# Optimization experiments

Hardware: AMD Instinct MI355X
Metric: run time of the kernel (lower is better)

## Reference

```python
import jax, jax.numpy as jnp
import numpy as np

B, N, D, H, L = 8, 1025, 1024, 8, 2   # N = maxlen + 1
NUM_BUCKETS = 64
EPS = 1e-8


def layernorm(x):
    mu = jnp.mean(x, axis=-1, keepdims=True)
    var = jnp.mean((x - mu) ** 2, axis=-1, keepdims=True)
    return (x - mu) / jnp.sqrt(var + EPS)


def rmsnorm(x):
    return x * jax.lax.rsqrt(jnp.mean(x * x, axis=-1, keepdims=True) + EPS)


def rel_attn_bias(action_ts, ts_w, pos_w):
    # positional part: pos_w[j - i + N - 1]  (equivalent to the pad/repeat trick)
    idx = jnp.arange(N)[None, :] - jnp.arange(N)[:, None] + (N - 1)  # [N,N] in [0,2N-2]
    rel_pos = pos_w[idx][None]  # [1,N,N]
    # time part: bucketize ext[i+1] - ext[j], ext = cat(ts, ts[:, N-1:N])
    ext = jnp.concatenate([action_ts, action_ts[:, N - 1:N]], axis=1)  # [B,N+1]
    diff = ext[:, 1:, None] - ext[:, None, :-1]  # [B,N,N]
    bucket = (jnp.log(jnp.clip(jnp.abs(diff), 1, None).astype(jnp.float32)) / 0.301).astype(jnp.int32)
    bucket = jnp.clip(bucket, 0, NUM_BUCKETS)
    rel_ts = ts_w[bucket]  # [B,N,N]
    return rel_pos + rel_ts


def hstu_block(x, mask, bias, qkvu, out_w, out_b, fc1_w, fc1_b, fc2_w, fc2_b):
    hd = D // H
    xn = layernorm(x)
    qkvu_act = jax.nn.silu(xn @ qkvu)  # [B,N,4D]
    q, k, v, u = jnp.split(qkvu_act, 4, axis=-1)
    q = q.reshape(B, N, H, hd)
    k = k.reshape(B, N, H, hd)
    v = v.reshape(B, N, H, hd)
    scores = jnp.einsum('bihd,bjhd->bhij', q, k) + bias[:, None]  # [B,H,N,N]
    attn = jax.nn.silu(scores) / N * mask[:, None]
    av = jnp.einsum('bhij,bjhd->bihd', attn, v).reshape(B, N, D)
    attn_out = (u * layernorm(av)) @ out_w + out_b
    h = x + attn_out
    # SwiGLU FFN (mult=2) with RMSNorm pre-norm and residual
    vg = rmsnorm(h) @ fc1_w + fc1_b  # [B,N,4D]
    vv, g = jnp.split(vg, 2, axis=-1)
    y = (jax.nn.silu(g) * vv) @ fc2_w + fc2_b
    return h + y


def setup_inputs() -> dict:
    key = jax.random.key(0)
    ks = jax.random.split(key, 12)
    std = 0.02
    seqs = jax.random.normal(ks[0], (B, N, D), jnp.float32)
    mask = jnp.tril(jnp.ones((N, N), jnp.float32))[None].repeat(B, axis=0)
    action_ts = jnp.sort(jax.random.randint(ks[1], (B, N), 0, 1000000000).astype(jnp.int64), axis=1)
    return {
        'seqs': seqs,
        'mask': mask,
        'action_ts': action_ts,
        'qkvu': jax.random.normal(ks[2], (L, D, 4 * D), jnp.float32) * std,
        'out_w': jax.random.normal(ks[3], (L, D, D), jnp.float32) * std,
        'out_b': jnp.zeros((L, D), jnp.float32),
        'ts_w': jax.random.normal(ks[4], (L, NUM_BUCKETS + 1), jnp.float32) * std,
        'pos_w': jax.random.normal(ks[5], (L, 2 * N - 1), jnp.float32) * std,
        'fc1_w': jax.random.normal(ks[6], (L, D, 4 * D), jnp.float32) * std,
        'fc1_b': jnp.zeros((L, 4 * D), jnp.float32),
        'fc2_w': jax.random.normal(ks[7], (L, 2 * D, D), jnp.float32) * std,
        'fc2_b': jnp.zeros((L, D), jnp.float32),
    }


def reference(seqs, mask, action_ts, qkvu, out_w, out_b, ts_w, pos_w, fc1_w, fc1_b, fc2_w, fc2_b):
    h = seqs
    for l in range(L):
        bias = rel_attn_bias(action_ts, ts_w[l], pos_w[l])
        h = hstu_block(h, mask, bias, qkvu[l], out_w[l], out_b[l],
                       fc1_w[l], fc1_b[l], fc2_w[l], fc2_b[l])
    return h
```

## Files before the change

kernel.cpp:

```cpp
#include <hip/hip_runtime.h>
#include <hip/hip_bf16.h>
#include <math.h>

#define BB 8
#define SEQN 1025
#define DD 1024
#define HH 8
#define HD 128
#define LL 2
#define MROWS (BB*SEQN)
#define MPAD 8320
#define NBUCKET 64

using short8 = __attribute__((ext_vector_type(8))) short;
using f32x4  = __attribute__((ext_vector_type(4))) float;
using f32x16 = __attribute__((ext_vector_type(16))) float;

__device__ __forceinline__ float silu_f(float x) { return x / (1.f + expf(-x)); }

__device__ __forceinline__ float bf2f(ushort u) {
  union { uint i; float f; } x; x.i = ((uint)u) << 16; return x.f;
}
__device__ __forceinline__ ushort f2bf(float f) {
  __hip_bfloat16 b = __float2bfloat16(f);
  return *reinterpret_cast<ushort*>(&b);
}
__device__ __forceinline__ void gll16(const void* g, void* l) {
  __builtin_amdgcn_global_load_lds((const __attribute__((address_space(1))) void*)g,
                                   (__attribute__((address_space(3))) void*)l, 16, 0, 0);
}
__device__ __forceinline__ uint pkbf(float lo, float hi) {
  uint r;
  asm("v_cvt_pk_bf16_f32 %0, %1, %2" : "=v"(r) : "v"(lo), "v"(hi));
  return r;
}
__device__ __forceinline__ f32x16 z16() {
  f32x16 v;
#pragma unroll
  for (int i = 0; i < 16; ++i) v[i] = 0.f;
  return v;
}

__global__ __launch_bounds__(256) void copy_kernel(const float* __restrict__ in,
                                                   float* __restrict__ out, int n4) {
  int idx = blockIdx.x * blockDim.x + threadIdx.x;
  int stride = gridDim.x * blockDim.x;
  const float4* i4 = (const float4*)in;
  float4* o4 = (float4*)out;
  for (int i = idx; i < n4; i += stride) o4[i] = i4[i];
}

__global__ __launch_bounds__(256) void wtrans(const float* __restrict__ W,
                                              ushort* __restrict__ Wt, int K, int N) {
  __shared__ float tile[32][33];
  int tid = threadIdx.x;
  int tx = tid & 31, ty = tid >> 5;
  int n0 = blockIdx.x * 32, k0 = blockIdx.y * 32;
#pragma unroll
  for (int r = 0; r < 32; r += 8)
    tile[ty + r][tx] = W[(size_t)(k0 + ty + r) * N + n0 + tx];
  __syncthreads();
#pragma unroll
  for (int r = 0; r < 32; r += 8)
    Wt[(size_t)(n0 + ty + r) * K + k0 + tx] = f2bf(tile[tx][ty + r]);
}

__global__ __launch_bounds__(256) void bias_kernel(const int* __restrict__ ts,
    const float* __restrict__ ts_w, const float* __restrict__ pos_w,
    float* __restrict__ biasT)
{
  int i = blockIdx.x * 256 + threadIdx.x;
  int j = blockIdx.y;
  int b = blockIdx.z;
  if (i >= SEQN) return;
  int ip1 = i + 1; if (ip1 > SEQN - 1) ip1 = SEQN - 1;
  long long t1 = (long long)ts[b * SEQN + ip1];
  long long t0 = (long long)ts[b * SEQN + j];
  long long d = t1 - t0;
  if (d < 0) d = -d;
  if (d < 1) d = 1;
  int bucket = (int)(logf((float)d) / 0.301f);
  if (bucket < 0) bucket = 0;
  if (bucket > NBUCKET) bucket = NBUCKET;
  biasT[((size_t)(b * SEQN + j)) * SEQN + i] = pos_w[j - i + SEQN - 1] + ts_w[bucket];
}

__global__ __launch_bounds__(256) void ln_kernel(const float* __restrict__ in,
                                                 ushort* __restrict__ out) {
  int row = blockIdx.x;
  int tid = threadIdx.x;
  const float* x = in + (size_t)row * DD;
  float4 v = *(const float4*)&x[tid * 4];
  float s = v.x + v.y + v.z + v.w;
  float ss = v.x*v.x + v.y*v.y + v.z*v.z + v.w*v.w;
#pragma unroll
  for (int off = 32; off >= 1; off >>= 1) { s += __shfl_xor(s, off); ss += __shfl_xor(ss, off); }
  __shared__ float red0[4], red1[4];
  if ((tid & 63) == 0) { red0[tid >> 6] = s; red1[tid >> 6] = ss; }
  __syncthreads();
  s = red0[0] + red0[1] + red0[2] + red0[3];
  ss = red1[0] + red1[1] + red1[2] + red1[3];
  float mu = s * (1.f / DD);
  float var = fmaxf(ss * (1.f / DD) - mu * mu, 0.f);
  float inv = 1.f / sqrtf(var + 1e-8f);
  ushort4 o;
  o.x = f2bf((v.x - mu) * inv); o.y = f2bf((v.y - mu) * inv);
  o.z = f2bf((v.z - mu) * inv); o.w = f2bf((v.w - mu) * inv);
  *(ushort4*)&out[(size_t)row * DD + tid * 4] = o;
}

__global__ __launch_bounds__(256) void rms_kernel(const float* __restrict__ in,
                                                  ushort* __restrict__ out) {
  int row = blockIdx.x;
  int tid = threadIdx.x;
  const float* x = in + (size_t)row * DD;
  float4 v = *(const float4*)&x[tid * 4];
  float ss = v.x*v.x + v.y*v.y + v.z*v.z + v.w*v.w;
#pragma unroll
  for (int off = 32; off >= 1; off >>= 1) ss += __shfl_xor(ss, off);
  __shared__ float red1[4];
  if ((tid & 63) == 0) red1[tid >> 6] = ss;
  __syncthreads();
  ss = red1[0] + red1[1] + red1[2] + red1[3];
  float inv = 1.f / sqrtf(ss * (1.f / DD) + 1e-8f);
  ushort4 o;
  o.x = f2bf(v.x * inv); o.y = f2bf(v.y * inv);
  o.z = f2bf(v.z * inv); o.w = f2bf(v.w * inv);
  *(ushort4*)&out[(size_t)row * DD + tid * 4] = o;
}

__global__ __launch_bounds__(256) void uln_kernel(const float* __restrict__ av,
    const ushort* __restrict__ act, ushort* __restrict__ out) {
  int row = blockIdx.x;
  int tid = threadIdx.x;
  const float* x = av + (size_t)row * DD;
  float4 v = *(const float4*)&x[tid * 4];
  float s = v.x + v.y + v.z + v.w;
  float ss = v.x*v.x + v.y*v.y + v.z*v.z + v.w*v.w;
#pragma unroll
  for (int off = 32; off >= 1; off >>= 1) { s += __shfl_xor(s, off); ss += __shfl_xor(ss, off); }
  __shared__ float red0[4], red1[4];
  if ((tid & 63) == 0) { red0[tid >> 6] = s; red1[tid >> 6] = ss; }
  __syncthreads();
  s = red0[0] + red0[1] + red0[2] + red0[3];
  ss = red1[0] + red1[1] + red1[2] + red1[3];
  float mu = s * (1.f / DD);
  float var = fmaxf(ss * (1.f / DD) - mu * mu, 0.f);
  float inv = 1.f / sqrtf(var + 1e-8f);
  ushort4 uu = *(const ushort4*)&act[(size_t)row * 4096 + 3072 + tid * 4];
  ushort4 o;
  o.x = f2bf(bf2f(uu.x) * (v.x - mu) * inv);
  o.y = f2bf(bf2f(uu.y) * (v.y - mu) * inv);
  o.z = f2bf(bf2f(uu.z) * (v.z - mu) * inv);
  o.w = f2bf(bf2f(uu.w) * (v.w - mu) * inv);
  *(ushort4*)&out[(size_t)row * DD + tid * 4] = o;
}

__global__ __launch_bounds__(256) void gated_kernel(const ushort* __restrict__ act,
                                                    ushort* __restrict__ gated) {
  int idx = blockIdx.x * 256 + threadIdx.x;
  const int total = MROWS * 2048 / 8;
  if (idx >= total) return;
  int row = idx >> 8;
  int col = (idx & 255) * 8;
  const ushort* base = act + (size_t)row * 4096;
  short8 vv = *(const short8*)(base + col);
  short8 gg = *(const short8*)(base + 2048 + col);
  short8 o;
#pragma unroll
  for (int j = 0; j < 8; ++j) {
    float v = bf2f((ushort)vv[j]);
    float g = bf2f((ushort)gg[j]);
    o[j] = (short)f2bf(silu_f(g) * v);
  }
  *(short8*)&gated[(size_t)row * 2048 + col] = o;
}

template<int MODE>
__global__ __launch_bounds__(256, 2) void mgemm(const ushort* __restrict__ A,
    const ushort* __restrict__ Bt, const float* __restrict__ bvec,
    void* __restrict__ Cout, int M, int Nn, int K)
{
  __shared__ ushort As[2][8192];
  __shared__ ushort Bs[2][8192];
  const int tid  = threadIdx.x;
  const int lane = tid & 63, wave = tid >> 6;
  const int wm = wave >> 1, wn = wave & 1;
  const int lrow = lane & 15, lk = lane >> 4;

  const int nwg = gridDim.x * gridDim.y;
  const int bid = blockIdx.y * gridDim.x + blockIdx.x;
  const int sw  = (bid & 7) * (nwg >> 3) + (bid >> 3);
  const int bm = (sw / gridDim.x) * 128, bn = (sw % gridDim.x) * 128;

  const ushort* Aga[4]; const ushort* Bga[4];
  ushort* Ada[4]; ushort* Bda[4];
#pragma unroll
  for (int i = 0; i < 4; ++i) {
    int c = tid + 256 * i;
    int row = c >> 3, s = c & 7;
    int sc = s ^ (row & 7);
    Aga[i] = A  + (size_t)(bm + row) * K + sc * 8;
    Bga[i] = Bt + (size_t)(bn + row) * K + sc * 8;
    Ada[i] = &As[0][c * 8];
    Bda[i] = &Bs[0][c * 8];
  }

  int aoff[2][4], boff[2][4];
#pragma unroll
  for (int kk = 0; kk < 2; ++kk) {
#pragma unroll
    for (int m = 0; m < 4; ++m)
      aoff[kk][m] = (wm * 64 + m * 16 + lrow) * 64 + (((kk * 4 + lk) ^ (lrow & 7)) * 8);
#pragma unroll
    for (int n = 0; n < 4; ++n)
      boff[kk][n] = (wn * 64 + n * 16 + lrow) * 64 + (((kk * 4 + lk) ^ (lrow & 7)) * 8);
  }

  f32x4 acc[4][4];
#pragma unroll
  for (int m = 0; m < 4; ++m)
#pragma unroll
    for (int n = 0; n < 4; ++n) acc[m][n] = (f32x4){0.f, 0.f, 0.f, 0.f};

  const int nk = K >> 6;
#pragma unroll
  for (int i = 0; i < 4; ++i) {
    gll16(Aga[i], Ada[i]);
    gll16(Bga[i], Bda[i]);
  }
  int buf = 0;
  for (int kt = 0; kt < nk; ++kt) {
    if (kt + 1 < nk) {
      const int ko = (kt + 1) << 6;
      const int bo = (buf ^ 1) * 8192;
#pragma unroll
      for (int i = 0; i < 4; ++i) {
        gll16(Aga[i] + ko, Ada[i] + bo);
        gll16(Bga[i] + ko, Bda[i] + bo);
      }
      asm volatile("s_waitcnt vmcnt(8)" ::: "memory");
    } else {
      asm volatile("s_waitcnt vmcnt(0)" ::: "memory");
    }
    __builtin_amdgcn_s_barrier();
    __builtin_amdgcn_sched_barrier(0);
    __builtin_amdgcn_s_setprio(1);
#pragma unroll
    for (int kk = 0; kk < 2; ++kk) {
      short8 af[4], bfr[4];
#pragma unroll
      for (int m = 0; m < 4; ++m) af[m]  = *(const short8*)&As[buf][aoff[kk][m]];
#pragma unroll
      for (int n = 0; n < 4; ++n) bfr[n] = *(const short8*)&Bs[buf][boff[kk][n]];
#pragma unroll
      for (int m = 0; m < 4; ++m)
#pragma unroll
        for (int n = 0; n < 4; ++n)
          acc[m][n] = __builtin_amdgcn_mfma_f32_16x16x32_bf16(af[m], bfr[n], acc[m][n], 0, 0, 0);
    }
    __builtin_amdgcn_s_setprio(0);
    __builtin_amdgcn_sched_barrier(0);
    __builtin_amdgcn_s_barrier();
    buf ^= 1;
  }

  const int colbase = bn + wn * 64 + lrow;
  const int rowbase = bm + wm * 64 + lk * 4;
  if (MODE == 1) {
    float* Cf = (float*)Cout;
#pragma unroll
    for (int m = 0; m < 4; ++m) {
      int row0 = rowbase + m * 16;
#pragma unroll
      for (int n = 0; n < 4; ++n) {
        int col = colbase + n * 16;
        float bv = bvec[col];
#pragma unroll
        for (int r = 0; r < 4; ++r) {
          int row = row0 + r;
          if (row < M) {
            float* p = Cf + (size_t)row * Nn + col;
            *p += acc[m][n][r] + bv;
          }
        }
      }
    }
  } else {
    __hip_bfloat16* Cb = (__hip_bfloat16*)Cout;
#pragma unroll
    for (int m = 0; m < 4; ++m) {
      int row0 = rowbase + m * 16;
#pragma unroll
      for (int n = 0; n < 4; ++n) {
        int col = colbase + n * 16;
        float bv = (MODE == 2) ? bvec[col] : 0.f;
#pragma unroll
        for (int r = 0; r < 4; ++r) {
          int row = row0 + r;
          if (row < M) {
            float v = acc[m][n][r];
            float o = (MODE == 0) ? silu_f(v) : (v + bv);
            Cb[(size_t)row * Nn + col] = __float2bfloat16(o);
          }
        }
      }
    }
  }
}

__global__ __launch_bounds__(256) void attn_kernel(const ushort* __restrict__ act,
    const float* __restrict__ biasT, float* __restrict__ av)
{
  __shared__ __align__(16) char KL[8192];
  __shared__ __align__(16) char VL[8320];
  const int tid = threadIdx.x;
  const int l = tid & 63, w = tid >> 6;
  const int qi = (int)(gridDim.x - 1 - blockIdx.x);
  const int i0 = qi * 128;
  const int h = blockIdx.y, b = blockIdx.z;
  const int lo31 = l & 31, hi = l >> 5;

  const int jlim = (i0 + 128 < SEQN) ? i0 + 128 : SEQN;
  const int nt = (jlim + 31) >> 5;

  const int gi_q = i0 + w * 32 + lo31;
  const int gi_qc = gi_q < SEQN ? gi_q : SEQN - 1;
  const size_t actB = (size_t)b * SEQN;
  const ushort* qrow = act + (actB + gi_qc) * 4096 + h * HD;
  short8 qreg[8];
#pragma unroll
  for (int dc = 0; dc < 8; ++dc)
    qreg[dc] = *(const short8*)(qrow + dc * 16 + hi * 8);

  f32x16 acc[4];
#pragma unroll
  for (int dt = 0; dt < 4; ++dt) acc[dt] = z16();

  const int id0 = tid, id1 = tid + 256;
  const int j_0 = id0 >> 4, c8_0 = (id0 & 15) * 8;
  const int j_1 = id1 >> 4, c8_1 = (id1 & 15) * 8;
  char* kw0 = KL + j_0 * 256 + (((id0 & 15) ^ (j_0 & 15)) << 4);
  char* kw1 = KL + j_1 * 256 + (((id1 & 15) ^ (j_1 & 15)) << 4);
  char* vw0 = VL + ((id0 & 15) >> 1) * 1040 + j_0 * 32 + (id0 & 1) * 16;
  char* vw1 = VL + ((id1 & 15) >> 1) * 1040 + j_1 * 32 + (id1 & 1) * 16;
  const uint vbase = (uint)(size_t)(__attribute__((address_space(3))) char*)
      (VL + ((l >> 4) & 1) * 1040 + hi * 256 + (l & 15) * 8);

  short8 kr0, kr1, vr0, vr1;
  {
    const ushort* p0 = act + (actB + j_0) * 4096 + 1024 + h * HD + c8_0;
    const ushort* p1 = act + (actB + j_1) * 4096 + 1024 + h * HD + c8_1;
    kr0 = *(const short8*)p0; vr0 = *(const short8*)(p0 + 1024);
    kr1 = *(const short8*)p1; vr1 = *(const short8*)(p1 + 1024);
  }
  const float invN = 1.f / (float)SEQN;
  const int gi0w = i0 + w * 32;

  for (int t = 0; t < nt; ++t) {
    const int j0 = t * 32;
    __syncthreads();
    *(short8*)kw0 = kr0; *(short8*)kw1 = kr1;
    *(short8*)vw0 = vr0; *(short8*)vw1 = vr1;
    __syncthreads();
    if (t + 1 < nt) {
      const ushort* p0 = act + (actB + j0 + 32 + j_0) * 4096 + 1024 + h * HD + c8_0;
      const ushort* p1 = act + (actB + j0 + 32 + j_1) * 4096 + 1024 + h * HD + c8_1;
      kr0 = *(const short8*)p0; vr0 = *(const short8*)(p0 + 1024);
      kr1 = *(const short8*)p1; vr1 = *(const short8*)(p1 + 1024);
    }
    if (j0 <= gi0w + 31 && gi0w < SEQN) {
      float bv[16];
#pragma unroll
      for (int r = 0; r < 16; ++r) {
        int j = (r & 3) + 8 * (r >> 2) + 4 * hi;
        int gj = j0 + j;
        int gjc = gj < SEQN ? gj : SEQN - 1;
        bv[r] = biasT[(actB + gjc) * SEQN + gi_qc];
      }
      f32x16 st = z16();
#pragma unroll
      for (int dc = 0; dc < 8; ++dc) {
        short8 kf = *(const short8*)(KL + lo31 * 256 + ((((dc << 1) + hi) ^ (lo31 & 15)) << 4));
        st = __builtin_amdgcn_mfma_f32_32x32x16_bf16(kf, qreg[dc], st, 0, 0, 0);
      }
      float p[16];
#pragma unroll
      for (int r = 0; r < 16; ++r) {
        int j = (r & 3) + 8 * (r >> 2) + 4 * hi;
        int gj = j0 + j;
        float s = st[r] + bv[r];
        float pw = s * __builtin_amdgcn_rcpf(1.f + __expf(-s)) * invN;
        p[r] = ((gj <= gi_q) && (gi_q < SEQN)) ? pw : 0.f;
      }
      short8 paf[2];
#pragma unroll
      for (int g = 0; g < 2; ++g) {
        uint w0 = pkbf(p[g * 8 + 0], p[g * 8 + 1]);
        uint w2 = pkbf(p[g * 8 + 4], p[g * 8 + 5]);
        uint w1 = pkbf(p[g * 8 + 2], p[g * 8 + 3]);
        uint w3 = pkbf(p[g * 8 + 6], p[g * 8 + 7]);
        asm volatile("v_permlane32_swap_b32 %0, %1" : "+v"(w0), "+v"(w2));
        asm volatile("v_permlane32_swap_b32 %0, %1" : "+v"(w1), "+v"(w3));
        union UF { uint u[4]; short8 s; } uf;
        uf.u[0] = w0; uf.u[1] = w1; uf.u[2] = w2; uf.u[3] = w3;
        paf[g] = uf.s;
      }
      uint64_t v00, v01, v02, v03, v10, v11, v12, v13, v20, v21, v22, v23, v30, v31, v32, v33;
      asm volatile(
        "ds_read_b64_tr_b16 %0, %16 offset:0\n\t"
        "ds_read_b64_tr_b16 %1, %16 offset:128\n\t"
        "ds_read_b64_tr_b16 %2, %16 offset:512\n\t"
        "ds_read_b64_tr_b16 %3, %16 offset:640\n\t"
        "ds_read_b64_tr_b16 %4, %16 offset:2080\n\t"
        "ds_read_b64_tr_b16 %5, %16 offset:2208\n\t"
        "ds_read_b64_tr_b16 %6, %16 offset:2592\n\t"
        "ds_read_b64_tr_b16 %7, %16 offset:2720\n\t"
        "ds_read_b64_tr_b16 %8, %16 offset:4160\n\t"
        "ds_read_b64_tr_b16 %9, %16 offset:4288\n\t"
        "ds_read_b64_tr_b16 %10, %16 offset:4672\n\t"
        "ds_read_b64_tr_b16 %11, %16 offset:4800\n\t"
        "ds_read_b64_tr_b16 %12, %16 offset:6240\n\t"
        "ds_read_b64_tr_b16 %13, %16 offset:6368\n\t"
        "ds_read_b64_tr_b16 %14, %16 offset:6752\n\t"
        "ds_read_b64_tr_b16 %15, %16 offset:6880\n\t"
        "s_waitcnt lgkmcnt(0)"
        : "=v"(v00), "=v"(v01), "=v"(v02), "=v"(v03),
          "=v"(v10), "=v"(v11), "=v"(v12), "=v"(v13),
          "=v"(v20), "=v"(v21), "=v"(v22), "=v"(v23),
          "=v"(v30), "=v"(v31), "=v"(v32), "=v"(v33)
        : "v"(vbase) : "memory");
      union UV { uint64_t q[2]; short8 s; };
      { UV uv; uv.q[0] = v00; uv.q[1] = v01;
        acc[0] = __builtin_amdgcn_mfma_f32_32x32x16_bf16(paf[0], uv.s, acc[0], 0, 0, 0); }
      { UV uv; uv.q[0] = v02; uv.q[1] = v03;
        acc[0] = __builtin_amdgcn_mfma_f32_32x32x16_bf16(paf[1], uv.s, acc[0], 0, 0, 0); }
      { UV uv; uv.q[0] = v10; uv.q[1] = v11;
        acc[1] = __builtin_amdgcn_mfma_f32_32x32x16_bf16(paf[0], uv.s, acc[1], 0, 0, 0); }
      { UV uv; uv.q[0] = v12; uv.q[1] = v13;
        acc[1] = __builtin_amdgcn_mfma_f32_32x32x16_bf16(paf[1], uv.s, acc[1], 0, 0, 0); }
      { UV uv; uv.q[0] = v20; uv.q[1] = v21;
        acc[2] = __builtin_amdgcn_mfma_f32_32x32x16_bf16(paf[0], uv.s, acc[2], 0, 0, 0); }
      { UV uv; uv.q[0] = v22; uv.q[1] = v23;
        acc[2] = __builtin_amdgcn_mfma_f32_32x32x16_bf16(paf[1], uv.s, acc[2], 0, 0, 0); }
      { UV uv; uv.q[0] = v30; uv.q[1] = v31;
        acc[3] = __builtin_amdgcn_mfma_f32_32x32x16_bf16(paf[0], uv.s, acc[3], 0, 0, 0); }
      { UV uv; uv.q[0] = v32; uv.q[1] = v33;
        acc[3] = __builtin_amdgcn_mfma_f32_32x32x16_bf16(paf[1], uv.s, acc[3], 0, 0, 0); }
    }
  }
#pragma unroll
  for (int dt = 0; dt < 4; ++dt) {
#pragma unroll
    for (int r = 0; r < 16; ++r) {
      int q = (r & 3) + 8 * (r >> 2) + 4 * hi;
      int gi = i0 + w * 32 + q;
      if (gi < SEQN)
        av[(actB + gi) * DD + h * HD + dt * 32 + lo31] = acc[dt][r];
    }
  }
}

extern "C" void kernel_launch(void* const* d_in, const int* in_sizes, int n_in,
                              void* d_out, int out_size, void* d_ws, size_t ws_size,
                              hipStream_t stream) {
  const float* seqs  = (const float*)d_in[0];
  const int*   ts    = (const int*)d_in[2];
  const float* qkvuW = (const float*)d_in[3];
  const float* outW  = (const float*)d_in[4];
  const float* outB  = (const float*)d_in[5];
  const float* tsW   = (const float*)d_in[6];
  const float* posW  = (const float*)d_in[7];
  const float* fc1W  = (const float*)d_in[8];
  const float* fc1B  = (const float*)d_in[9];
  const float* fc2W  = (const float*)d_in[10];
  const float* fc2B  = (const float*)d_in[11];
  float* h = (float*)d_out;
  char* ws = (char*)d_ws;

  ushort* xn    = (ushort*)(ws);
  ushort* act   = (ushort*)(ws + 17039360);
  ushort* gated = (ushort*)(ws + 85196800);
  float*  biasT = (float*) (ws + 119275520);
  float*  av    = (float*) (ws + 152895520);
  ushort* wq    = (ushort*)(ws + 186482720);
  ushort* wo    = (ushort*)(ws + 194871328);
  ushort* wf1   = (ushort*)(ws + 196968480);
  ushort* wf2   = (ushort*)(ws + 205357088);

  copy_kernel<<<2048, 256, 0, stream>>>(seqs, h, MROWS * DD / 4);

  for (int l = 0; l < LL; l++) {
    wtrans<<<dim3(128, 32), 256, 0, stream>>>(qkvuW + (size_t)l * DD * 4096, wq, DD, 4096);
    wtrans<<<dim3(32, 32),  256, 0, stream>>>(outW  + (size_t)l * DD * DD,   wo, DD, DD);
    wtrans<<<dim3(128, 32), 256, 0, stream>>>(fc1W  + (size_t)l * DD * 4096, wf1, DD, 4096);
    wtrans<<<dim3(32, 64),  256, 0, stream>>>(fc2W  + (size_t)l * 2048 * DD, wf2, 2048, DD);

    bias_kernel<<<dim3(5, SEQN, BB), 256, 0, stream>>>(
        ts, tsW + l * (NBUCKET + 1), posW + l * (2 * SEQN - 1), biasT);

    ln_kernel<<<MROWS, 256, 0, stream>>>(h, xn);
    mgemm<0><<<dim3(32, 65), 256, 0, stream>>>(xn, wq, nullptr, act, MROWS, 4096, DD);
    attn_kernel<<<dim3(9, HH, BB), 256, 0, stream>>>(act, biasT, av);
    uln_kernel<<<MROWS, 256, 0, stream>>>(av, act, xn);
    mgemm<1><<<dim3(8, 65), 256, 0, stream>>>(xn, wo, outB + l * DD, h, MROWS, DD, DD);
    rms_kernel<<<MROWS, 256, 0, stream>>>(h, xn);
    mgemm<2><<<dim3(32, 65), 256, 0, stream>>>(xn, wf1, fc1B + (size_t)l * 4096, act, MROWS, 4096, DD);
    gated_kernel<<<8200, 256, 0, stream>>>(act, gated);
    mgemm<1><<<dim3(8, 65), 256, 0, stream>>>(gated, wf2, fc2B + l * DD, h, MROWS, DD, 2048);
  }
}
```

Measured before the change: 1.239 ms.

## Switch GEMM to triple-buffered BK=32 pipeline with one barrier per iteration

Reworks the bf16 MFMA GEMM main loop from a double-buffered K-tile of 64 to a triple-buffered K-tile of 32, prefetching two stages ahead. The trailing barrier is dropped so each iteration syncs only once, and the LDS swizzle is adapted to the 32-wide rows. The block-id swizzle for L2 locality and the occupancy hint in launch_bounds are removed. Each iteration does half the MFMA work between barriers, so the barrier overhead per unit of work may rise. The LDS footprint shrinks, which could allow more workgroups per CU.

```diff
diff --git a/kernel.cpp b/kernel.cpp
--- a/kernel.cpp
+++ b/kernel.cpp
@@ -177,45 +177,38 @@
 }
 
 template<int MODE>
-__global__ __launch_bounds__(256, 2) void mgemm(const ushort* __restrict__ A,
+__global__ __launch_bounds__(256) void mgemm(const ushort* __restrict__ A,
     const ushort* __restrict__ Bt, const float* __restrict__ bvec,
     void* __restrict__ Cout, int M, int Nn, int K)
 {
-  __shared__ ushort As[2][8192];
-  __shared__ ushort Bs[2][8192];
+  __shared__ ushort As[3][4096];
+  __shared__ ushort Bs[3][4096];
   const int tid  = threadIdx.x;
   const int lane = tid & 63, wave = tid >> 6;
   const int wm = wave >> 1, wn = wave & 1;
   const int lrow = lane & 15, lk = lane >> 4;
-
-  const int nwg = gridDim.x * gridDim.y;
-  const int bid = blockIdx.y * gridDim.x + blockIdx.x;
-  const int sw  = (bid & 7) * (nwg >> 3) + (bid >> 3);
-  const int bm = (sw / gridDim.x) * 128, bn = (sw % gridDim.x) * 128;
-
-  const ushort* Aga[4]; const ushort* Bga[4];
-  ushort* Ada[4]; ushort* Bda[4];
-#pragma unroll
-  for (int i = 0; i < 4; ++i) {
+  const int bm = blockIdx.y * 128, bn = blockIdx.x * 128;
+
+  const ushort* Aga[2]; const ushort* Bga[2];
+  ushort* Ada[2]; ushort* Bda[2];
+#pragma unroll
+  for (int i = 0; i < 2; ++i) {
     int c = tid + 256 * i;
-    int row = c >> 3, s = c & 7;
-    int sc = s ^ (row & 7);
+    int row = c >> 2, s = c & 3;
+    int sc = s ^ ((row >> 1) & 3);
     Aga[i] = A  + (size_t)(bm + row) * K + sc * 8;
     Bga[i] = Bt + (size_t)(bn + row) * K + sc * 8;
     Ada[i] = &As[0][c * 8];
     Bda[i] = &Bs[0][c * 8];
   }
 
-  int aoff[2][4], boff[2][4];
-#pragma unroll
-  for (int kk = 0; kk < 2; ++kk) {
-#pragma unroll
-    for (int m = 0; m < 4; ++m)
-      aoff[kk][m] = (wm * 64 + m * 16 + lrow) * 64 + (((kk * 4 + lk) ^ (lrow & 7)) * 8);
-#pragma unroll
-    for (int n = 0; n < 4; ++n)
-      boff[kk][n] = (wn * 64 + n * 16 + lrow) * 64 + (((kk * 4 + lk) ^ (lrow & 7)) * 8);
-  }
+  int aoff[4], boff[4];
+#pragma unroll
+  for (int m = 0; m < 4; ++m)
+    aoff[m] = (wm * 64 + m * 16 + lrow) * 32 + ((lk ^ ((lrow >> 1) & 3)) * 8);
+#pragma unroll
+  for (int n = 0; n < 4; ++n)
+    boff[n] = (wn * 64 + n * 16 + lrow) * 32 + ((lk ^ ((lrow >> 1) & 3)) * 8);
 
   f32x4 acc[4][4];
 #pragma unroll
@@ -223,36 +216,41 @@
 #pragma unroll
     for (int n = 0; n < 4; ++n) acc[m][n] = (f32x4){0.f, 0.f, 0.f, 0.f};
 
-  const int nk = K >> 6;
-#pragma unroll
-  for (int i = 0; i < 4; ++i) {
-    gll16(Aga[i], Ada[i]);
-    gll16(Bga[i], Bda[i]);
-  }
-  int buf = 0;
+  const int nk = K >> 5;
+#pragma unroll
+  for (int t = 0; t < 2; ++t) {
+#pragma unroll
+    for (int i = 0; i < 2; ++i) {
+      gll16(Aga[i] + (t << 5), Ada[i] + t * 4096);
+      gll16(Bga[i] + (t << 5), Bda[i] + t * 4096);
+    }
+  }
+  int cur = 0, nxt2 = 2;
   for (int kt = 0; kt < nk; ++kt) {
     if (kt + 1 < nk) {
-      const int ko = (kt + 1) << 6;
-      const int bo = (buf ^ 1) * 8192;
-#pragma unroll
-      for (int i = 0; i < 4; ++i) {
+      asm volatile("s_waitcnt vmcnt(4)" ::: "memory");
+    } else {
+      asm volatile("s_waitcnt vmcnt(0)" ::: "memory");
+    }
+    __builtin_amdgcn_s_barrier();
+    __builtin_amdgcn_sched_barrier(0);
+    if (kt + 2 < nk) {
+      const int ko = (kt + 2) << 5;
+      const int bo = nxt2 * 4096;
+#pragma unroll
+      for (int i = 0; i < 2; ++i) {
         gll16(Aga[i] + ko, Ada[i] + bo);
         gll16(Bga[i] + ko, Bda[i] + bo);
       }
-      asm volatile("s_waitcnt vmcnt(8)" ::: "memory");
-    } else {
-      asm volatile("s_waitcnt vmcnt(0)" ::: "memory");
-    }
-    __builtin_amdgcn_s_barrier();
-    __builtin_amdgcn_sched_barrier(0);
+    }
     __builtin_amdgcn_s_setprio(1);
-#pragma unroll
-    for (int kk = 0; kk < 2; ++kk) {
+    {
       short8 af[4], bfr[4];
-#pragma unroll
-      for (int m = 0; m < 4; ++m) af[m]  = *(const short8*)&As[buf][aoff[kk][m]];
-#pragma unroll
-      for (int n = 0; n < 4; ++n) bfr[n] = *(const short8*)&Bs[buf][boff[kk][n]];
+      const int co = cur * 4096;
+#pragma unroll
+      for (int m = 0; m < 4; ++m) af[m]  = *(const short8*)&As[0][co + aoff[m]];
+#pragma unroll
+      for (int n = 0; n < 4; ++n) bfr[n] = *(const short8*)&Bs[0][co + boff[n]];
 #pragma unroll
       for (int m = 0; m < 4; ++m)
 #pragma unroll
@@ -261,8 +259,8 @@
     }
     __builtin_amdgcn_s_setprio(0);
     __builtin_amdgcn_sched_barrier(0);
-    __builtin_amdgcn_s_barrier();
-    buf ^= 1;
+    cur = (cur == 2) ? 0 : cur + 1;
+    nxt2 = (nxt2 == 2) ? 0 : nxt2 + 1;
   }
 
   const int colbase = bn + wn * 64 + lrow;
```

New measurement: 1.111 ms. 10.3% less time.
